# Optimization experiments

Measured on AMD Instinct MI355X. Metric: run time of the kernel, lower is better.

## Reference

```python
import jax, jax.numpy as jnp
import numpy as np

K = 1.0        # Lorentz curvature parameter
SQRT_K = 1.0
B, E, T = 128, 64, 2048
F1, D, F2, NC = 16, 2, 32, 4


def linner(u, v):
    # Lorentz inner product <u,v>_L over the last axis (time component first)
    return -u[..., :1] * v[..., :1] + jnp.sum(u[..., 1:] * v[..., 1:], axis=-1, keepdims=True)


def add_time(space):
    # manifold.add_time / projx: time = sqrt(K + ||space||^2)
    t = jnp.sqrt(K + jnp.sum(space * space, axis=-1, keepdims=True))
    return jnp.concatenate([t, space], axis=-1)


def conv2d(x, w, padding, groups=1):
    return jax.lax.conv_general_dilated(
        x, w, window_strides=(1, 1), padding=padding,
        dimension_numbers=('NCHW', 'OIHW', 'NCHW'), feature_group_count=groups)


def bn2d(x, gamma, beta, eps=1e-3):
    # BatchNorm2d (training-mode batch statistics, eps=0.001)
    mean = jnp.mean(x, axis=(0, 2, 3), keepdims=True)
    var = jnp.var(x, axis=(0, 2, 3), keepdims=True)
    return (x - mean) * jax.lax.rsqrt(var + eps) * gamma.reshape(1, -1, 1, 1) + beta.reshape(1, -1, 1, 1)


def avgpool_w(x, k=4):
    # torch AvgPool2d((1,k), stride=k), floor mode
    Wo = x.shape[-1] // k
    return jnp.mean(x[..., :Wo * k].reshape(x.shape[:-1] + (Wo, k)), axis=-1)


def lorentz_bn(x, s, eps=1e-5):
    # AdaMom-style Riemannian batch norm on the hyperboloid (eta=1 -> pure batch stats,
    # learn_mean=False -> target mean is origin, learn_std=True -> learnable scale s).
    C = x.shape[-1]
    o = jnp.zeros((C,), x.dtype).at[0].set(SQRT_K)                      # origin
    avg = jnp.mean(x, axis=0, keepdims=True)
    mu = SQRT_K * avg / jnp.sqrt(jnp.maximum(-linner(avg, avg), 1e-8))  # batch centroid
    xin = -linner(x, mu)                                                # >= K on manifold
    dist = SQRT_K * jnp.arccosh(jnp.maximum(xin / K, 1.0 + 1e-7))
    u = x - (xin / K) * mu                                              # log_mu direction
    v = dist * u / jnp.sqrt(jnp.maximum(linner(u, u), 1e-8))            # log_mu(x)
    var = jnp.mean(dist * dist, axis=0, keepdims=True)                  # scalar dispersion
    v = v + (linner(o, v) / (K - linner(mu, o))) * (mu + o)             # PT mu -> origin
    v = v * (s.reshape(1, 1, -1, 1) / jnp.sqrt(var + eps))
    n = jnp.sqrt(jnp.maximum(linner(v, v), 1e-9))
    return jnp.cosh(n / SQRT_K) * o + SQRT_K * jnp.sinh(n / SQRT_K) * v / n  # exp_origin


def lorentz_avgpool_w(x, k=4):
    # window mean followed by Lorentz centroid renormalization
    Bb, H, W, C = x.shape
    Wo = W // k
    avg = jnp.mean(x[:, :, :Wo * k, :].reshape(Bb, H, Wo, k, C), axis=3)
    return SQRT_K * avg / jnp.sqrt(jnp.maximum(-linner(avg, avg), 1e-8))


def lorentz_flatten(x):
    Bb, H, W, C = x.shape
    t = x[..., 0].reshape(Bb, -1)
    s = x[..., 1:].reshape(Bb, -1)
    t_new = jnp.sqrt(jnp.maximum(jnp.sum(t * t, axis=-1, keepdims=True) - (H * W - 1) * K, 1e-8))
    return jnp.concatenate([t_new, s], axis=-1)


def lorentz_mlr(x, a, z):
    inv = 1.0 / SQRT_K
    norm_z = jnp.linalg.norm(z, axis=-1)                                  # (NC,)
    w_t = jnp.sinh(inv * a) * norm_z
    beta = jnp.sqrt(jnp.maximum((jnp.cosh(inv * a) * norm_z) ** 2 - w_t ** 2, 1e-8))
    alpha = -x[:, :1] * w_t[None, :] + jnp.cosh(inv * a)[None, :] * (x[:, 1:] @ z.T)
    d = SQRT_K * jnp.abs(jnp.arcsinh(inv * alpha / beta[None, :]))
    return jnp.sign(alpha) * beta[None, :] * d


def setup_inputs():
    key = jax.random.key(0)
    ks = jax.random.split(key, 8)
    Cin = F1 * D + 1   # 33
    Cout = F2 + 1      # 33
    feat = F2 * 128    # flattened space dim: W 2049 -> 512 -> 513 -> 128
    return {
        'inputs': jax.random.normal(ks[0], (B, E, T), jnp.float32),
        'domains': jax.random.randint(ks[1], (B,), 0, 4, jnp.int32),
        'conv1_w': jax.random.normal(ks[2], (F1, 1, 1, 32), jnp.float32) / np.float32(np.sqrt(32.0)),
        'bn1_gamma': jnp.ones((F1,), jnp.float32),
        'bn1_beta': jnp.zeros((F1,), jnp.float32),
        'conv2_w': jax.random.normal(ks[3], (F1 * D, 1, E, 1), jnp.float32) / np.float32(np.sqrt(E)),
        'bn2_gamma': jnp.ones((F1 * D,), jnp.float32),
        'bn2_beta': jnp.zeros((F1 * D,), jnp.float32),
        'ec1_w': jax.random.normal(ks[4], (F1 * D, 1, 1, 16), jnp.float32) / np.float32(np.sqrt(16.0)),
        'lc1_w': jax.random.normal(ks[5], (Cout, Cin), jnp.float32) / np.float32(np.sqrt(Cin)),
        'bn_s': jnp.ones((513,), jnp.float32),
        'mlr_a': jax.random.normal(ks[6], (NC,), jnp.float32) * 0.01,
        'mlr_z': jax.random.normal(ks[7], (NC, feat), jnp.float32) * 0.01,
    }


def reference(inputs, domains, conv1_w, bn1_gamma, bn1_beta, conv2_w, bn2_gamma, bn2_beta,
              ec1_w, lc1_w, bn_s, mlr_a, mlr_z):
    x = inputs[:, None, :, :]                           # (B,1,E,T)
    x = conv2d(x, conv1_w, [(0, 0), (16, 16)])          # (B,16,64,2049)
    x = bn2d(x, bn1_gamma, bn1_beta)
    x = conv2d(x, conv2_w, [(0, 0), (0, 0)], groups=F1) # (B,32,1,2049) depthwise over electrodes
    x = bn2d(x, bn2_gamma, bn2_beta)
    x = jax.nn.elu(x)
    x = avgpool_w(x)                                    # (B,32,1,512)  (dropout = eval no-op)
    x = conv2d(x, ec1_w, [(0, 0), (8, 8)], groups=F1 * D)  # (B,32,1,513)
    x = jnp.transpose(x, (0, 2, 3, 1))                  # (B,1,513,32) channels-last
    x = x / (jnp.linalg.norm(x, axis=-1, keepdims=True) + 1e-8)
    x = add_time(x)                                     # projx(pad(x, (1,0))) -> (B,1,513,33)
    # LorentzConv2d 1x1 (kernel_len=1): clamp time, linear, recompute time from space output
    pre = jnp.concatenate([jnp.maximum(x[..., :1], SQRT_K), x[..., 1:]], axis=-1)
    y = jnp.einsum('bhwi,oi->bhwo', pre, lc1_w)
    x = add_time(y[..., 1:])
    x = lorentz_bn(x, bn_s)
    x = add_time(jax.nn.elu(x[..., 1:]))                # LorentzeLU
    x = lorentz_avgpool_w(x)                            # (B,1,128,33)
    feats = lorentz_flatten(x)                          # (B, 4097)
    logits = lorentz_mlr(feats, mlr_a, mlr_z)           # (B, 4)
    return logits, feats
```

## Files before the change

### kernel.cpp

```cpp
#include <hip/hip_runtime.h>
#include <math.h>

#define BB 128
#define EE 64
#define TT 2048
#define C2 32
#define W1 2049
#define WPW 512
#define FEAT 4096
#define NBLK 1024

#define OFF_P    ((size_t)0)
#define OFF_X2   ((size_t)4194304)
#define OFF_PSUM ((size_t)8388608)
#define OFF_PSQ  ((size_t)8421376)
#define OFF_SS   ((size_t)8454144)
#define OFF_Y    ((size_t)8454208)
#define OFF_ZZ   ((size_t)9502784)
#define OFF_QSQ  ((size_t)11599936)

__device__ __forceinline__ unsigned short f2b(float f) {
    unsigned int u = __float_as_uint(f);
    u += 0x7FFFu + ((u >> 16) & 1u);
    return (unsigned short)(u >> 16);
}
__device__ __forceinline__ float b2f(unsigned short s) {
    return __uint_as_float(((unsigned int)s) << 16);
}

__global__ __launch_bounds__(256) void k_p(const float* __restrict__ in,
        const float* __restrict__ w2, unsigned short* __restrict__ P) {
    int b = blockIdx.y, t0 = blockIdx.x * 256, tid = threadIdx.x;
    __shared__ unsigned short li[64][256];
    __shared__ float lw2s[32][64];
    const float* ib = in + (size_t)b * EE * TT + t0;
    for (int j = tid; j < 64 * 64; j += 256) {
        int e = j >> 6, q = j & 63;
        float4 v = *(const float4*)(ib + e * TT + q * 4);
        li[e][q * 4 + 0] = f2b(v.x); li[e][q * 4 + 1] = f2b(v.y);
        li[e][q * 4 + 2] = f2b(v.z); li[e][q * 4 + 3] = f2b(v.w);
    }
    for (int j = tid; j < 2048; j += 256) lw2s[j >> 6][j & 63] = w2[j];
    __syncthreads();
    int cg = tid >> 6, colg = tid & 63;
    int c8 = cg * 8;
    float acc[4][8];
#pragma unroll
    for (int x = 0; x < 4; x++)
#pragma unroll
        for (int jj = 0; jj < 8; jj++) acc[x][jj] = 0.f;
    for (int e = 0; e < 64; e += 2) {
        uint2 r0 = *(const uint2*)&li[e][colg * 4];
        uint2 r1 = *(const uint2*)&li[e + 1][colg * 4];
        float v0[4], v1[4];
        v0[0] = __uint_as_float(r0.x << 16); v0[1] = __uint_as_float(r0.x & 0xFFFF0000u);
        v0[2] = __uint_as_float(r0.y << 16); v0[3] = __uint_as_float(r0.y & 0xFFFF0000u);
        v1[0] = __uint_as_float(r1.x << 16); v1[1] = __uint_as_float(r1.x & 0xFFFF0000u);
        v1[2] = __uint_as_float(r1.y << 16); v1[3] = __uint_as_float(r1.y & 0xFFFF0000u);
#pragma unroll
        for (int jj = 0; jj < 8; jj++) {
            float2 wv = *(const float2*)&lw2s[c8 + jj][e];
#pragma unroll
            for (int x = 0; x < 4; x++) {
                acc[x][jj] = fmaf(wv.x, v0[x], acc[x][jj]);
                acc[x][jj] = fmaf(wv.y, v1[x], acc[x][jj]);
            }
        }
    }
    unsigned short* Pb = P + (size_t)b * C2 * TT + t0 + colg * 4;
#pragma unroll
    for (int jj = 0; jj < 8; jj++) {
        int c = c8 + jj;
        uint2 o;
        o.x = (unsigned int)f2b(acc[0][jj]) | ((unsigned int)f2b(acc[1][jj]) << 16);
        o.y = (unsigned int)f2b(acc[2][jj]) | ((unsigned int)f2b(acc[3][jj]) << 16);
        *(uint2*)(Pb + (size_t)c * TT) = o;
    }
}

__global__ __launch_bounds__(256) void k_cs(const unsigned short* __restrict__ P,
        const float* __restrict__ w1, const float* __restrict__ g1,
        unsigned short* __restrict__ x2, float* __restrict__ psum, float* __restrict__ psq) {
    int bx = blockIdx.x, b = blockIdx.y, w0 = bx * 256, tid = threadIdx.x;
    __shared__ unsigned short lp[32][288];
    __shared__ float lw1[16][32];
    __shared__ float lds_s[32], lds_q[32];
    const unsigned short* Pb = P + (size_t)b * C2 * TT;
    for (int j = tid; j < 32 * 72; j += 256) {
        int c = j / 72, g4 = j % 72;
        int t = w0 - 16 + g4 * 4;
        uint2 v = make_uint2(0u, 0u);
        if (t >= 0 && t + 3 < TT) v = *(const uint2*)(Pb + (size_t)c * TT + t);
        *(uint2*)&lp[c][g4 * 4] = v;
    }
    for (int j = tid; j < 512; j += 256) {
        int g = j >> 5;
        float sgn = (g1[g] < 0.f) ? -1.f : 1.f;
        lw1[g][j & 31] = w1[j] * sgn;
    }
    __syncthreads();
    for (int r = 0; r < 8; r++) {
        int task = r * 256 + tid;
        int c = task >> 6;
        int wq = task & 63;
        int wbase = wq * 4;
        float win[36];
#pragma unroll
        for (int i = 0; i < 9; i++) {
            uint2 v = *(const uint2*)&lp[c][wbase + i * 4];
            win[i * 4 + 0] = __uint_as_float(v.x << 16);
            win[i * 4 + 1] = __uint_as_float(v.x & 0xFFFF0000u);
            win[i * 4 + 2] = __uint_as_float(v.y << 16);
            win[i * 4 + 3] = __uint_as_float(v.y & 0xFFFF0000u);
        }
        const float* wc = lw1[c >> 1];
        float ls = 0.f, lq = 0.f;
        float accs[4];
#pragma unroll
        for (int i = 0; i < 4; i++) {
            float acc = 0.f;
#pragma unroll
            for (int k = 0; k < 32; k++) acc = fmaf(wc[k], win[i + k], acc);
            accs[i] = acc;
            ls += acc; lq = fmaf(acc, acc, lq);
        }
        uint2 o;
        o.x = (unsigned int)f2b(accs[0]) | ((unsigned int)f2b(accs[1]) << 16);
        o.y = (unsigned int)f2b(accs[2]) | ((unsigned int)f2b(accs[3]) << 16);
        *(uint2*)(x2 + ((size_t)b * C2 + c) * TT + w0 + wbase) = o;
#pragma unroll
        for (int d = 1; d < 64; d <<= 1) {
            ls += __shfl_xor(ls, d);
            lq += __shfl_xor(lq, d);
        }
        if ((tid & 63) == 0) { lds_s[c] = ls; lds_q[c] = lq; }
    }
    __syncthreads();
    if (bx == 7 && tid < 32) {
        const float* wc = lw1[tid >> 1];
        float acc = 0.f;
#pragma unroll
        for (int k = 0; k < 16; k++) acc = fmaf(wc[k], b2f(lp[tid][256 + k]), acc);
        lds_s[tid] += acc;
        lds_q[tid] += acc * acc;
    }
    __syncthreads();
    if (tid < 32) {
        int blk = b * 8 + bx;
        psum[tid * NBLK + blk] = lds_s[tid];
        psq[tid * NBLK + blk]  = lds_q[tid];
    }
}

__global__ __launch_bounds__(64) void k_bn2fin(
        const float* __restrict__ psum, const float* __restrict__ psq,
        const float* __restrict__ gamma, const float* __restrict__ beta,
        float* __restrict__ ss) {
    int c = blockIdx.x, l = threadIdx.x;
    float s = 0.f, q = 0.f;
    for (int j = l; j < NBLK; j += 64) { s += psum[c * NBLK + j]; q += psq[c * NBLK + j]; }
#pragma unroll
    for (int d = 1; d < 64; d <<= 1) { s += __shfl_xor(s, d); q += __shfl_xor(q, d); }
    if (l == 0) {
        float n = (float)(BB * W1);
        float m = s / n;
        float var = q / n - m * m;
        float sc = gamma[c] * rsqrtf(var + 1e-3f);
        ss[c] = sc;
        ss[32 + c] = beta[c] - m * sc;
    }
}

__global__ __launch_bounds__(256) void k_pool2(
        const unsigned short* __restrict__ x2, const float* __restrict__ ss,
        unsigned short* __restrict__ y) {
    int idx = blockIdx.x * 256 + threadIdx.x;
    int wp = idx & 511;
    int bc = idx >> 9;
    int c = bc & 31;
    uint2 v = *(const uint2*)(x2 + (size_t)bc * TT + wp * 4);
    float sc = ss[c], sh = ss[32 + c];
    float a, s = 0.f;
    a = fmaf(sc, __uint_as_float(v.x << 16), sh);        s += (a > 0.f) ? a : expm1f(a);
    a = fmaf(sc, __uint_as_float(v.x & 0xFFFF0000u), sh); s += (a > 0.f) ? a : expm1f(a);
    a = fmaf(sc, __uint_as_float(v.y << 16), sh);        s += (a > 0.f) ? a : expm1f(a);
    a = fmaf(sc, __uint_as_float(v.y & 0xFFFF0000u), sh); s += (a > 0.f) ? a : expm1f(a);
    y[idx] = f2b(s * 0.25f);
}

__global__ __launch_bounds__(256) void k_ec1(
        const unsigned short* __restrict__ y, const float* __restrict__ ew,
        float* __restrict__ zz) {
    int b = blockIdx.y, w0 = blockIdx.x * 64;
    int tid = threadIdx.x, c = tid & 31, wl = tid >> 5;
    __shared__ unsigned short ly[32][84];
    __shared__ float lew[32][16];
    const unsigned short* yb = y + (size_t)b * C2 * WPW;
    for (int j = tid; j < 32 * 20; j += 256) {
        int cc = j / 20, g4 = j % 20;
        int t = w0 - 8 + g4 * 4;
        uint2 v = make_uint2(0u, 0u);
        if (t >= 0 && t + 3 < WPW) v = *(const uint2*)(yb + (size_t)cc * WPW + t);
        *(uint2*)&ly[cc][g4 * 4] = v;
    }
    for (int j = tid; j < 512; j += 256) lew[j >> 4][j & 15] = ew[j];
    __syncthreads();
    float win[24];
#pragma unroll
    for (int i = 0; i < 6; i++) {
        uint2 v = *(const uint2*)&ly[c][wl * 8 + i * 4];
        win[i * 4 + 0] = __uint_as_float(v.x << 16);
        win[i * 4 + 1] = __uint_as_float(v.x & 0xFFFF0000u);
        win[i * 4 + 2] = __uint_as_float(v.y << 16);
        win[i * 4 + 3] = __uint_as_float(v.y & 0xFFFF0000u);
    }
    const float* wc = lew[c];
#pragma unroll
    for (int i = 0; i < 8; i++) {
        float acc = 0.f;
#pragma unroll
        for (int k = 0; k < 16; k++) acc = fmaf(wc[k], win[i + k], acc);
        zz[((size_t)(w0 + wl * 8 + i) * BB + b) * C2 + c] = acc;
    }
}

__global__ __launch_bounds__(512) void k_tail(
        const float* __restrict__ zz, const float* __restrict__ lc1,
        const float* __restrict__ bs, float* __restrict__ outp,
        float* __restrict__ qsq) {
    int wp = blockIdx.x;
    int tid = threadIdx.x;
    int j = tid >> 7;
    int b = tid & 127;
    int w = wp * 4 + j;
    __shared__ float lw[1089];
    __shared__ float wsum[4][2][33];
    __shared__ float vred[4][2];
    __shared__ float lavg[128][33];
    for (int i = tid; i < 1089; i += 512) lw[i] = lc1[i];
    float* lz = &lavg[0][0];
    for (int i = tid; i < 128 * 33; i += 512) lz[i] = 0.f;
    __syncthreads();
    float x[33];
    {
        float xin[32];
        float ssq = 0.f;
        const float* zp = zz + ((size_t)w * BB + b) * C2;
#pragma unroll
        for (int i = 0; i < 32; i += 4) {
            float4 v = *(const float4*)(zp + i);
            xin[i] = v.x; xin[i + 1] = v.y; xin[i + 2] = v.z; xin[i + 3] = v.w;
        }
#pragma unroll
        for (int i = 0; i < 32; i++) ssq = fmaf(xin[i], xin[i], ssq);
        float inv = 1.f / (sqrtf(ssq) + 1e-8f);
        float s2 = 0.f;
#pragma unroll
        for (int i = 0; i < 32; i++) { xin[i] *= inv; s2 = fmaf(xin[i], xin[i], s2); }
        float t = sqrtf(1.f + s2);
        float pre0 = fmaxf(t, 1.f);
        float sy = 0.f;
        for (int o = 1; o < 33; o++) {
            const float* wr = lw + o * 33;
            float a = wr[0] * pre0;
#pragma unroll
            for (int i = 0; i < 32; i++) a = fmaf(wr[1 + i], xin[i], a);
            x[o] = a;
            sy = fmaf(a, a, sy);
        }
        x[0] = sqrtf(1.f + sy);
    }
    float mu[33];
#pragma unroll
    for (int ch = 0; ch < 33; ch++) {
        float s = x[ch];
        s += __shfl_xor(s, 1);  s += __shfl_xor(s, 2);  s += __shfl_xor(s, 4);
        s += __shfl_xor(s, 8);  s += __shfl_xor(s, 16); s += __shfl_xor(s, 32);
        mu[ch] = s;
    }
    int wv = b >> 6;
    if ((b & 63) == 0) {
#pragma unroll
        for (int ch = 0; ch < 33; ch++) wsum[j][wv][ch] = mu[ch];
    }
    __syncthreads();
#pragma unroll
    for (int ch = 0; ch < 33; ch++) mu[ch] = (wsum[j][0][ch] + wsum[j][1][ch]) * (1.f / 128.f);
    float a0 = mu[0], sp = 0.f;
#pragma unroll
    for (int i = 1; i < 33; i++) sp = fmaf(mu[i], mu[i], sp);
    float rd = rsqrtf(fmaxf(a0 * a0 - sp, 1e-8f));
#pragma unroll
    for (int ch = 0; ch < 33; ch++) mu[ch] *= rd;
    float xin = x[0] * mu[0];
#pragma unroll
    for (int i = 1; i < 33; i++) xin -= x[i] * mu[i];
    float dist = acoshf(fmaxf(xin, 1.f + 1e-7f));
    float dq = dist * dist;
    dq += __shfl_xor(dq, 1);  dq += __shfl_xor(dq, 2);  dq += __shfl_xor(dq, 4);
    dq += __shfl_xor(dq, 8);  dq += __shfl_xor(dq, 16); dq += __shfl_xor(dq, 32);
    if ((b & 63) == 0) vred[j][wv] = dq;
    __syncthreads();
    float var = (vred[j][0] + vred[j][1]) * (1.f / 128.f);
#pragma unroll
    for (int ch = 0; ch < 33; ch++) x[ch] = x[ch] - xin * mu[ch];
    float lu = -x[0] * x[0];
#pragma unroll
    for (int i = 1; i < 33; i++) lu = fmaf(x[i], x[i], lu);
    float f = dist * rsqrtf(fmaxf(lu, 1e-8f));
#pragma unroll
    for (int ch = 0; ch < 33; ch++) x[ch] *= f;
    float corr = -x[0] / (1.f + mu[0]);
    x[0] += corr * (mu[0] + 1.f);
#pragma unroll
    for (int i = 1; i < 33; i++) x[i] = fmaf(corr, mu[i], x[i]);
    float scb = bs[w] * rsqrtf(var + 1e-5f);
#pragma unroll
    for (int ch = 0; ch < 33; ch++) x[ch] *= scb;
    float nn = -x[0] * x[0];
#pragma unroll
    for (int i = 1; i < 33; i++) nn = fmaf(x[i], x[i], nn);
    float n = sqrtf(fmaxf(nn, 1e-9f));
    float shn = sinhf(n) / n;
    float sg = 0.f;
#pragma unroll
    for (int i = 1; i < 33; i++) {
        float e = shn * x[i];
        e = (e > 0.f) ? e : expm1f(e);
        x[i] = e;
        sg = fmaf(e, e, sg);
    }
    x[0] = sqrtf(1.f + sg);
    for (int jj = 0; jj < 4; jj++) {
        if (j == jj) {
#pragma unroll
            for (int ch = 0; ch < 33; ch++) lavg[b][ch] += x[ch];
        }
        __syncthreads();
    }
    if (tid < 128) {
        int bb2 = tid;
        float avg[33];
#pragma unroll
        for (int ch = 0; ch < 33; ch++) avg[ch] = lavg[bb2][ch] * 0.25f;
        float sp2 = 0.f;
#pragma unroll
        for (int i = 1; i < 33; i++) sp2 = fmaf(avg[i], avg[i], sp2);
        float l = avg[0] * avg[0] - sp2;
        float rd2 = rsqrtf(fmaxf(l, 1e-8f));
        float q0 = avg[0] * rd2;
        float* fb = outp + 512 + (size_t)bb2 * 4097;
#pragma unroll
        for (int i = 1; i < 33; i++) fb[1 + wp * 32 + (i - 1)] = avg[i] * rd2;
        qsq[bb2 * 128 + wp] = q0 * q0;
    }
}

__global__ __launch_bounds__(256) void k_mlr2(
        const float* __restrict__ qsq, const float* __restrict__ z,
        const float* __restrict__ a, float* __restrict__ outp) {
    int b = blockIdx.x, tid = threadIdx.x;
    __shared__ float red[4][8];
    __shared__ float tnsh;
    if (tid < 64) {
        float s = qsq[b * 128 + tid] + qsq[b * 128 + 64 + tid];
#pragma unroll
        for (int d = 1; d < 64; d <<= 1) s += __shfl_xor(s, d);
        if (tid == 0) tnsh = sqrtf(fmaxf(s - 127.f, 1e-8f));
    }
    __syncthreads();
    float tn = tnsh;
    const float* fs = outp + 512 + (size_t)b * 4097 + 1;
    float sdot[4] = {0.f, 0.f, 0.f, 0.f}, sq[4] = {0.f, 0.f, 0.f, 0.f};
    for (int i = tid * 4; i < FEAT; i += 1024) {
        float f0 = fs[i], f1 = fs[i + 1], f2 = fs[i + 2], f3 = fs[i + 3];
#pragma unroll
        for (int c = 0; c < 4; c++) {
            float4 zv = *(const float4*)(z + c * FEAT + i);
            sdot[c] = fmaf(f0, zv.x, sdot[c]); sdot[c] = fmaf(f1, zv.y, sdot[c]);
            sdot[c] = fmaf(f2, zv.z, sdot[c]); sdot[c] = fmaf(f3, zv.w, sdot[c]);
            sq[c] = fmaf(zv.x, zv.x, sq[c]); sq[c] = fmaf(zv.y, zv.y, sq[c]);
            sq[c] = fmaf(zv.z, zv.z, sq[c]); sq[c] = fmaf(zv.w, zv.w, sq[c]);
        }
    }
#pragma unroll
    for (int d = 1; d < 64; d <<= 1) {
#pragma unroll
        for (int c = 0; c < 4; c++) {
            sdot[c] += __shfl_xor(sdot[c], d);
            sq[c]   += __shfl_xor(sq[c], d);
        }
    }
    int wv = tid >> 6;
    if ((tid & 63) == 0) {
#pragma unroll
        for (int c = 0; c < 4; c++) { red[wv][c] = sdot[c]; red[wv][4 + c] = sq[c]; }
    }
    __syncthreads();
    if (tid == 0) {
        outp[512 + (size_t)b * 4097] = tn;
#pragma unroll
        for (int c = 0; c < 4; c++) {
            float dot = red[0][c] + red[1][c] + red[2][c] + red[3][c];
            float qz  = red[0][4 + c] + red[1][4 + c] + red[2][4 + c] + red[3][4 + c];
            float nz = sqrtf(qz);
            float ca = coshf(a[c]), sa = sinhf(a[c]);
            float wt = sa * nz;
            float cb = ca * nz;
            float bb = sqrtf(fmaxf(cb * cb - wt * wt, 1e-8f));
            float alpha = fmaf(-tn, wt, ca * dot);
            float d = fabsf(asinhf(alpha / bb));
            float sg = (alpha > 0.f) ? 1.f : ((alpha < 0.f) ? -1.f : 0.f);
            outp[b * 4 + c] = sg * bb * d;
        }
    }
}

extern "C" void kernel_launch(void* const* d_in, const int* in_sizes, int n_in,
                              void* d_out, int out_size, void* d_ws, size_t ws_size,
                              hipStream_t stream) {
    const float* in   = (const float*)d_in[0];
    const float* w1   = (const float*)d_in[2];
    const float* g1   = (const float*)d_in[3];
    const float* w2   = (const float*)d_in[5];
    const float* g2   = (const float*)d_in[6];
    const float* b2   = (const float*)d_in[7];
    const float* ew   = (const float*)d_in[8];
    const float* lc1  = (const float*)d_in[9];
    const float* bs   = (const float*)d_in[10];
    const float* mlra = (const float*)d_in[11];
    const float* mlrz = (const float*)d_in[12];
    float* out = (float*)d_out;
    float* ws = (float*)d_ws;

    unsigned short* P  = (unsigned short*)(ws + OFF_P);
    unsigned short* X2 = (unsigned short*)(ws + OFF_X2);
    float* PSUM = ws + OFF_PSUM;
    float* PSQ  = ws + OFF_PSQ;
    float* SS   = ws + OFF_SS;
    unsigned short* Y = (unsigned short*)(ws + OFF_Y);
    float* ZZ   = ws + OFF_ZZ;
    float* QSQ  = ws + OFF_QSQ;

    k_p<<<dim3(8, 128), 256, 0, stream>>>(in, w2, P);
    k_cs<<<dim3(8, 128), 256, 0, stream>>>(P, w1, g1, X2, PSUM, PSQ);
    k_bn2fin<<<32, 64, 0, stream>>>(PSUM, PSQ, g2, b2, SS);
    k_pool2<<<8192, 256, 0, stream>>>(X2, SS, Y);
    k_ec1<<<dim3(8, 128), 256, 0, stream>>>(Y, ew, ZZ);
    k_tail<<<128, 512, 0, stream>>>(ZZ, lc1, bs, out, QSQ);
    k_mlr2<<<128, 256, 0, stream>>>(QSQ, mlrz, mlra, out);
}
```

Before: 211.1 us.

## Fuse BN-ELU-avgpool into the ec1 conv kernel and vectorize tail weight loads

Merges the pooling kernel into the depthwise ec1 convolution. Each block now loads a raw x2 tile with halo, applies BN scale/shift, ELU and 4-wide average pooling in shared memory, then runs the 16-tap conv. This drops one launch and the round trip of the intermediate Y tensor through global memory, and keeps the pooled values in fp32 instead of rounding to bf16. The cost is that halo pooled values are recomputed per block. The tail kernel also splits the Lorentz linear weights into time and space arrays so the space part can be read as float4 from shared memory.

```diff
diff --git a/kernel.cpp b/kernel.cpp
--- a/kernel.cpp
+++ b/kernel.cpp
@@ -15,9 +15,8 @@
 #define OFF_PSUM ((size_t)8388608)
 #define OFF_PSQ  ((size_t)8421376)
 #define OFF_SS   ((size_t)8454144)
-#define OFF_Y    ((size_t)8454208)
-#define OFF_ZZ   ((size_t)9502784)
-#define OFF_QSQ  ((size_t)11599936)
+#define OFF_ZZ   ((size_t)8454208)
+#define OFF_QSQ  ((size_t)10551360)
 
 __device__ __forceinline__ unsigned short f2b(float f) {
     unsigned int u = __float_as_uint(f);
@@ -171,56 +170,63 @@
     }
 }
 
-__global__ __launch_bounds__(256) void k_pool2(
+__global__ __launch_bounds__(256) void k_mid(
         const unsigned short* __restrict__ x2, const float* __restrict__ ss,
-        unsigned short* __restrict__ y) {
-    int idx = blockIdx.x * 256 + threadIdx.x;
-    int wp = idx & 511;
-    int bc = idx >> 9;
-    int c = bc & 31;
-    uint2 v = *(const uint2*)(x2 + (size_t)bc * TT + wp * 4);
-    float sc = ss[c], sh = ss[32 + c];
-    float a, s = 0.f;
-    a = fmaf(sc, __uint_as_float(v.x << 16), sh);        s += (a > 0.f) ? a : expm1f(a);
-    a = fmaf(sc, __uint_as_float(v.x & 0xFFFF0000u), sh); s += (a > 0.f) ? a : expm1f(a);
-    a = fmaf(sc, __uint_as_float(v.y << 16), sh);        s += (a > 0.f) ? a : expm1f(a);
-    a = fmaf(sc, __uint_as_float(v.y & 0xFFFF0000u), sh); s += (a > 0.f) ? a : expm1f(a);
-    y[idx] = f2b(s * 0.25f);
-}
-
-__global__ __launch_bounds__(256) void k_ec1(
-        const unsigned short* __restrict__ y, const float* __restrict__ ew,
-        float* __restrict__ zz) {
-    int b = blockIdx.y, w0 = blockIdx.x * 64;
-    int tid = threadIdx.x, c = tid & 31, wl = tid >> 5;
-    __shared__ unsigned short ly[32][84];
-    __shared__ float lew[32][16];
-    const unsigned short* yb = y + (size_t)b * C2 * WPW;
-    for (int j = tid; j < 32 * 20; j += 256) {
-        int cc = j / 20, g4 = j % 20;
-        int t = w0 - 8 + g4 * 4;
+        const float* __restrict__ ew, float* __restrict__ zz) {
+    int b = blockIdx.y, w0 = blockIdx.x * 64, tid = threadIdx.x;
+    __shared__ unsigned short lx[32][324];
+    __shared__ float ly[32][82];
+    __shared__ float lss[64];
+    __shared__ float lew[32][17];
+    const unsigned short* xb = x2 + (size_t)b * C2 * TT;
+    int base_t = 4 * w0 - 32;
+    for (int it = 0; it < 10; it++) {
+        int idx = it * 256 + tid;
+        int c = idx / 80, q = idx - c * 80;
+        int t0 = base_t + q * 4;
         uint2 v = make_uint2(0u, 0u);
-        if (t >= 0 && t + 3 < WPW) v = *(const uint2*)(yb + (size_t)cc * WPW + t);
-        *(uint2*)&ly[cc][g4 * 4] = v;
-    }
+        if (t0 >= 0 && t0 <= TT - 4) v = *(const uint2*)(xb + (size_t)c * TT + t0);
+        *(uint2*)&lx[c][q * 4] = v;
+    }
+    if (tid < 64) lss[tid] = ss[tid];
     for (int j = tid; j < 512; j += 256) lew[j >> 4][j & 15] = ew[j];
     __syncthreads();
+    for (int it = 0; it < 10; it++) {
+        int idx = it * 256 + tid;
+        int c = idx & 31, j2 = idx >> 5;
+        int ty = w0 - 8 + j2;
+        float r = 0.f;
+        if (ty >= 0 && ty < WPW) {
+            uint2 v = *(const uint2*)&lx[c][j2 * 4];
+            float sc = lss[c], sh = lss[32 + c];
+            float a0 = fmaf(sc, __uint_as_float(v.x << 16), sh);
+            float a1 = fmaf(sc, __uint_as_float(v.x & 0xFFFF0000u), sh);
+            float a2 = fmaf(sc, __uint_as_float(v.y << 16), sh);
+            float a3 = fmaf(sc, __uint_as_float(v.y & 0xFFFF0000u), sh);
+            r = ((a0 > 0.f) ? a0 : expm1f(a0)) + ((a1 > 0.f) ? a1 : expm1f(a1))
+              + ((a2 > 0.f) ? a2 : expm1f(a2)) + ((a3 > 0.f) ? a3 : expm1f(a3));
+            r *= 0.25f;
+        }
+        ly[c][j2] = r;
+    }
+    __syncthreads();
+    int c = tid & 31, wl = tid >> 5;
     float win[24];
 #pragma unroll
-    for (int i = 0; i < 6; i++) {
-        uint2 v = *(const uint2*)&ly[c][wl * 8 + i * 4];
-        win[i * 4 + 0] = __uint_as_float(v.x << 16);
-        win[i * 4 + 1] = __uint_as_float(v.x & 0xFFFF0000u);
-        win[i * 4 + 2] = __uint_as_float(v.y << 16);
-        win[i * 4 + 3] = __uint_as_float(v.y & 0xFFFF0000u);
-    }
-    const float* wc = lew[c];
+    for (int m = 0; m < 12; m++) {
+        float2 v = *(const float2*)&ly[c][wl * 8 + m * 2];
+        win[m * 2] = v.x; win[m * 2 + 1] = v.y;
+    }
+    float wc[16];
+#pragma unroll
+    for (int k = 0; k < 16; k++) wc[k] = lew[c][k];
+    float* zb = zz + ((size_t)(w0 + wl * 8) * BB + b) * C2 + c;
 #pragma unroll
     for (int i = 0; i < 8; i++) {
         float acc = 0.f;
 #pragma unroll
         for (int k = 0; k < 16; k++) acc = fmaf(wc[k], win[i + k], acc);
-        zz[((size_t)(w0 + wl * 8 + i) * BB + b) * C2 + c] = acc;
+        zb[(size_t)i * BB * C2] = acc;
     }
 }
 
@@ -233,11 +239,16 @@
     int j = tid >> 7;
     int b = tid & 127;
     int w = wp * 4 + j;
-    __shared__ float lw[1089];
+    __shared__ float lws[33][32];
+    __shared__ float lwt[33];
     __shared__ float wsum[4][2][33];
     __shared__ float vred[4][2];
     __shared__ float lavg[128][33];
-    for (int i = tid; i < 1089; i += 512) lw[i] = lc1[i];
+    for (int i = tid; i < 1089; i += 512) {
+        int o = i / 33, ii = i - o * 33;
+        float v = lc1[i];
+        if (ii == 0) lwt[o] = v; else lws[o][ii - 1] = v;
+    }
     float* lz = &lavg[0][0];
     for (int i = tid; i < 128 * 33; i += 512) lz[i] = 0.f;
     __syncthreads();
@@ -261,10 +272,15 @@
         float pre0 = fmaxf(t, 1.f);
         float sy = 0.f;
         for (int o = 1; o < 33; o++) {
-            const float* wr = lw + o * 33;
-            float a = wr[0] * pre0;
-#pragma unroll
-            for (int i = 0; i < 32; i++) a = fmaf(wr[1 + i], xin[i], a);
+            float a = lwt[o] * pre0;
+#pragma unroll
+            for (int q4 = 0; q4 < 8; q4++) {
+                float4 wv = *(const float4*)&lws[o][q4 * 4];
+                a = fmaf(wv.x, xin[q4 * 4 + 0], a);
+                a = fmaf(wv.y, xin[q4 * 4 + 1], a);
+                a = fmaf(wv.z, xin[q4 * 4 + 2], a);
+                a = fmaf(wv.w, xin[q4 * 4 + 3], a);
+            }
             x[o] = a;
             sy = fmaf(a, a, sy);
         }
@@ -292,10 +308,10 @@
     float rd = rsqrtf(fmaxf(a0 * a0 - sp, 1e-8f));
 #pragma unroll
     for (int ch = 0; ch < 33; ch++) mu[ch] *= rd;
-    float xin = x[0] * mu[0];
-#pragma unroll
-    for (int i = 1; i < 33; i++) xin -= x[i] * mu[i];
-    float dist = acoshf(fmaxf(xin, 1.f + 1e-7f));
+    float xin2 = x[0] * mu[0];
+#pragma unroll
+    for (int i = 1; i < 33; i++) xin2 -= x[i] * mu[i];
+    float dist = acoshf(fmaxf(xin2, 1.f + 1e-7f));
     float dq = dist * dist;
     dq += __shfl_xor(dq, 1);  dq += __shfl_xor(dq, 2);  dq += __shfl_xor(dq, 4);
     dq += __shfl_xor(dq, 8);  dq += __shfl_xor(dq, 16); dq += __shfl_xor(dq, 32);
@@ -303,7 +319,7 @@
     __syncthreads();
     float var = (vred[j][0] + vred[j][1]) * (1.f / 128.f);
 #pragma unroll
-    for (int ch = 0; ch < 33; ch++) x[ch] = x[ch] - xin * mu[ch];
+    for (int ch = 0; ch < 33; ch++) x[ch] = x[ch] - xin2 * mu[ch];
     float lu = -x[0] * x[0];
 #pragma unroll
     for (int i = 1; i < 33; i++) lu = fmaf(x[i], x[i], lu);
@@ -438,15 +454,13 @@
     float* PSUM = ws + OFF_PSUM;
     float* PSQ  = ws + OFF_PSQ;
     float* SS   = ws + OFF_SS;
-    unsigned short* Y = (unsigned short*)(ws + OFF_Y);
     float* ZZ   = ws + OFF_ZZ;
     float* QSQ  = ws + OFF_QSQ;
 
     k_p<<<dim3(8, 128), 256, 0, stream>>>(in, w2, P);
     k_cs<<<dim3(8, 128), 256, 0, stream>>>(P, w1, g1, X2, PSUM, PSQ);
     k_bn2fin<<<32, 64, 0, stream>>>(PSUM, PSQ, g2, b2, SS);
-    k_pool2<<<8192, 256, 0, stream>>>(X2, SS, Y);
-    k_ec1<<<dim3(8, 128), 256, 0, stream>>>(Y, ew, ZZ);
+    k_mid<<<dim3(8, 128), 256, 0, stream>>>(X2, SS, ew, ZZ);
     k_tail<<<128, 512, 0, stream>>>(ZZ, lc1, bs, out, QSQ);
     k_mlr2<<<128, 256, 0, stream>>>(QSQ, mlrz, mlra, out);
 }
```

Result: no change. 208.9 us (-1.1%).
